# Kernel tuning notes

Measured on AMD Instinct MI355X. Metric: run time of the kernel, lower is better.

## Reference

```python
import jax, jax.numpy as jnp
import numpy as np
from jax import lax

B, N, D, H, T = 32, 128, 512, 512, 31
INI = 0.01


def setup_inputs() -> dict:
    key = jax.random.key(0)
    ks = jax.random.split(key, 16)
    xav_dh = float(np.sqrt(2.0 / (D + H)))
    xav_hh = float(np.sqrt(2.0 / (H + H)))
    u = lambda k, s, a: jax.random.uniform(k, s, jnp.float32, -a, a)
    return {
        "attn_mem": jax.random.normal(ks[0], (B, N, D), jnp.float32),
        "mem_sizes": jax.random.randint(ks[1], (B,), 64, N + 1),
        "lstm_in": jax.random.normal(ks[2], (B, T, D), jnp.float32),
        "init_h": u(ks[3], (1, H), INI),
        "init_c": u(ks[4], (1, H), INI),
        "init_i": u(ks[5], (D,), 0.1),
        "w_ih": jax.random.normal(ks[6], (4 * H, D), jnp.float32) * xav_dh,
        "w_hh": jax.random.normal(ks[7], (4 * H, H), jnp.float32) * xav_hh,
        "b_ih": u(ks[8], (4 * H,), INI),
        "b_hh": u(ks[9], (4 * H,), INI),
        "attn_wm": jax.random.normal(ks[10], (D, H), jnp.float32) * xav_dh,
        "attn_wq": jax.random.normal(ks[11], (H, H), jnp.float32) * xav_hh,
        "attn_v": u(ks[12], (H,), INI),
        "hop_wm": jax.random.normal(ks[13], (D, H), jnp.float32) * xav_dh,
        "hop_wq": jax.random.normal(ks[14], (H, H), jnp.float32) * xav_hh,
        "hop_v": u(ks[15], (H,), INI),
    }


def _attention_score(feat, query, v, w):
    # feat: [B,N,H], query: [B,Tq,H] -> [B,Tq,N]
    q = jnp.einsum("bth,hk->btk", query, w)
    s = jnp.tanh(feat[:, None, :, :] + q[:, :, None, :])  # [B,Tq,N,H]
    return jnp.einsum("btnh,h->btn", s, v)


def _attention(feat, query, v, w, mask):
    score = _attention_score(feat, query, v, w)
    score = jnp.where(mask[:, None, :], score, -1e18)
    norm = jax.nn.softmax(score, axis=-1)
    return jnp.einsum("btn,bnh->bth", norm, feat)


def _lstm(x, h0, c0, w_ih, w_hh, b_ih, b_hh):
    # x: [T,B,D]; h0,c0: [B,H]; pytorch gate order i,f,g,o
    def step(carry, xt):
        h, c = carry
        g = xt @ w_ih.T + h @ w_hh.T + b_ih + b_hh
        i, f, gg, o = jnp.split(g, 4, axis=-1)
        c = jax.nn.sigmoid(f) * c + jax.nn.sigmoid(i) * jnp.tanh(gg)
        h = jax.nn.sigmoid(o) * jnp.tanh(c)
        return (h, c), h
    _, ys = lax.scan(step, (h0, c0), x)
    return ys  # [T,B,H]


def reference(attn_mem, mem_sizes, lstm_in, init_h, init_c, init_i,
              w_ih, w_hh, b_ih, b_hh, attn_wm, attn_wq, attn_v,
              hop_wm, hop_wq, hop_v, n_hop=1):
    bs, n, d = attn_mem.shape
    attn_feat = attn_mem @ attn_wm  # [B,N,H]
    hop_feat = attn_mem @ hop_wm   # [B,N,H]
    h0 = jnp.broadcast_to(init_h[0], (bs, init_h.shape[1]))
    c0 = jnp.broadcast_to(init_c[0], (bs, init_c.shape[1]))
    x = jnp.concatenate([jnp.broadcast_to(init_i, (bs, 1, d)), lstm_in], axis=1)
    query = _lstm(jnp.transpose(x, (1, 0, 2)), h0, c0, w_ih, w_hh, b_ih, b_hh)
    query = jnp.transpose(query, (1, 0, 2))  # [B,Tq,H]
    mask = jnp.arange(n)[None, :] < mem_sizes[:, None]  # [B,N]
    for _ in range(n_hop):
        query = _attention(hop_feat, query, hop_v, hop_wq, mask)
    return _attention_score(attn_feat, query, attn_v, attn_wq)
```

## Files before the change

kernel.cpp:

```cpp
#include <hip/hip_runtime.h>

typedef unsigned short u16;
typedef unsigned long long u64;
typedef __bf16 bf16x8 __attribute__((ext_vector_type(8)));
typedef float f32x4 __attribute__((ext_vector_type(4)));

__device__ __forceinline__ float b2f(u16 u) {
    unsigned int x = ((unsigned int)u) << 16;
    return __builtin_bit_cast(float, x);
}
__device__ __forceinline__ u16 f2b(float f) {
    unsigned int u = __builtin_bit_cast(unsigned int, f);
    unsigned int r = (u + 0x7FFFu + ((u >> 16) & 1u)) >> 16;
    return (u16)r;
}
__device__ __forceinline__ unsigned int pack2(float a, float b) {
    return (unsigned int)f2b(a) | ((unsigned int)f2b(b) << 16);
}
__device__ __forceinline__ float fast_rcp(float x) { return __builtin_amdgcn_rcpf(x); }
__device__ __forceinline__ float fast_tanh(float x) {
    float e = __expf(2.f * x);
    return 1.f - 2.f * fast_rcp(e + 1.f);
}
__device__ __forceinline__ float fast_sig(float x) {
    float e = __expf(-x);
    return fast_rcp(1.f + e);
}

#define FLAG_STRIDE 32

__launch_bounds__(256)
__global__ void k_prep(const float* __restrict__ attn_mem, u16* __restrict__ amem_bf,
                       const float* __restrict__ w_ih, u16* __restrict__ wih_bf,
                       const float* __restrict__ w_hh, u16* __restrict__ whh_bf,
                       const float* __restrict__ lstm_in, const float* __restrict__ init_i,
                       u16* __restrict__ xfull,
                       const float* s0, const float* s1, const float* s2, const float* s3,
                       u16* d0, u16* d1, u16* d2, u16* d3,
                       unsigned int* __restrict__ flags) {
    __shared__ float tile[32][33];
    int bid = blockIdx.x;
    int tid = threadIdx.x;
    if (bid == 0 && tid < 64)
        __hip_atomic_store(&flags[tid * FLAG_STRIDE], 0u, __ATOMIC_RELAXED,
                           __HIP_MEMORY_SCOPE_AGENT);
    if (bid < 4096) {
        const float* s;
        u16* d;
        int i;
        if (bid < 2048) { s = attn_mem; d = amem_bf; i = bid * 256 + tid; }
        else if (bid < 3072) { s = w_ih; d = wih_bf; i = (bid - 2048) * 256 + tid; }
        else { s = w_hh; d = whh_bf; i = (bid - 3072) * 256 + tid; }
        float4 a = ((const float4*)s)[i];
        uint2 p;
        p.x = pack2(a.x, a.y);
        p.y = pack2(a.z, a.w);
        ((uint2*)d)[i] = p;
    } else if (bid < 4608) {
        int idx = (bid - 4096) * 256 + tid;
        int c = idx & 127;
        int t = (idx >> 7) & 31;
        int b = idx >> 12;
        const float4* src = (t == 0) ? ((const float4*)init_i) + c
                                     : ((const float4*)lstm_in) + ((b * 31 + (t - 1)) * 128 + c);
        float4 a = *src;
        uint2 p;
        p.x = pack2(a.x, a.y);
        p.y = pack2(a.z, a.w);
        ((uint2*)xfull)[idx] = p;
    } else {
        int local = bid - 4608;
        int z = local >> 8, rem = local & 255;
        int by = (rem >> 4) * 32, bx = (rem & 15) * 32;
        const float* s;
        u16* d;
        switch (z) {
            case 0: s = s0; d = d0; break;
            case 1: s = s1; d = d1; break;
            case 2: s = s2; d = d2; break;
            default: s = s3; d = d3; break;
        }
        int tx = tid & 31, ty = tid >> 5;
        for (int i = 0; i < 32; i += 8) tile[ty + i][tx] = s[(by + ty + i) * 512 + bx + tx];
        __syncthreads();
        for (int i = 0; i < 32; i += 8) d[(bx + ty + i) * 512 + by + tx] = f2b(tile[tx][ty + i]);
    }
}

template <bool BF16OUT>
__launch_bounds__(256)
__global__ void k_gemm(const u16* __restrict__ A, const u16* __restrict__ Bt,
                       void* __restrict__ Cv, int GN,
                       const float* __restrict__ bias1, const float* __restrict__ bias2) {
    __shared__ u16 As[64][40];
    __shared__ u16 Bs[64][40];
    int m0 = blockIdx.y * 64, n0 = blockIdx.x * 64;
    int tid = threadIdx.x;
    int lane = tid & 63, w = tid >> 6;
    int wm = w >> 1, wn = w & 1;
    int l15 = lane & 15, quad = lane >> 4;
    f32x4 acc[2][2] = {};
    int ar = tid >> 2, ac = (tid & 3) * 8;
    const u16* Ap = A + (m0 + ar) * 512 + ac;
    const u16* Bp = Bt + (n0 + ar) * 512 + ac;
    for (int kt = 0; kt < 16; ++kt) {
        uint4 av = *(const uint4*)(Ap + kt * 32);
        uint4 bv = *(const uint4*)(Bp + kt * 32);
        __syncthreads();
        *(uint4*)&As[ar][ac] = av;
        *(uint4*)&Bs[ar][ac] = bv;
        __syncthreads();
        bf16x8 a0 = *(const bf16x8*)&As[wm * 32 + l15][quad * 8];
        bf16x8 a1 = *(const bf16x8*)&As[wm * 32 + 16 + l15][quad * 8];
        bf16x8 b0 = *(const bf16x8*)&Bs[wn * 32 + l15][quad * 8];
        bf16x8 b1 = *(const bf16x8*)&Bs[wn * 32 + 16 + l15][quad * 8];
        acc[0][0] = __builtin_amdgcn_mfma_f32_16x16x32_bf16(a0, b0, acc[0][0], 0, 0, 0);
        acc[0][1] = __builtin_amdgcn_mfma_f32_16x16x32_bf16(a0, b1, acc[0][1], 0, 0, 0);
        acc[1][0] = __builtin_amdgcn_mfma_f32_16x16x32_bf16(a1, b0, acc[1][0], 0, 0, 0);
        acc[1][1] = __builtin_amdgcn_mfma_f32_16x16x32_bf16(a1, b1, acc[1][1], 0, 0, 0);
    }
    for (int ai = 0; ai < 2; ++ai)
        for (int bi = 0; bi < 2; ++bi) {
            int row = m0 + wm * 32 + ai * 16 + quad * 4;
            int col = n0 + wn * 32 + bi * 16 + l15;
            float bias = 0.f;
            if (bias1) bias = bias1[col] + bias2[col];
            if constexpr (BF16OUT) {
                u16* C = (u16*)Cv;
                for (int r = 0; r < 4; ++r) C[(row + r) * GN + col] = f2b(acc[ai][bi][r] + bias);
            } else {
                float* C = (float*)Cv;
                for (int r = 0; r < 4; ++r) C[(row + r) * GN + col] = acc[ai][bi][r] + bias;
            }
        }
}

__launch_bounds__(256)
__global__ void k_feat(const u16* __restrict__ A,
                       const u16* __restrict__ B0, const u16* __restrict__ B1,
                       u16* __restrict__ C0, u16* __restrict__ C1) {
    __shared__ u16 As[64][40];
    __shared__ u16 Bs[64][40];
    int by = blockIdx.y;
    const u16* Bt;
    u16* C;
    int m0;
    if (by < 64) { Bt = B0; C = C0; m0 = by * 64; }
    else { Bt = B1; C = C1; m0 = (by - 64) * 64; }
    int n0 = blockIdx.x * 64;
    int tid = threadIdx.x;
    int lane = tid & 63, w = tid >> 6;
    int wm = w >> 1, wn = w & 1;
    int l15 = lane & 15, quad = lane >> 4;
    f32x4 acc[2][2] = {};
    int ar = tid >> 2, ac = (tid & 3) * 8;
    const u16* Ap = A + (m0 + ar) * 512 + ac;
    const u16* Bp = Bt + (n0 + ar) * 512 + ac;
    for (int kt = 0; kt < 16; ++kt) {
        uint4 av = *(const uint4*)(Ap + kt * 32);
        uint4 bv = *(const uint4*)(Bp + kt * 32);
        __syncthreads();
        *(uint4*)&As[ar][ac] = av;
        *(uint4*)&Bs[ar][ac] = bv;
        __syncthreads();
        bf16x8 a0 = *(const bf16x8*)&As[wm * 32 + l15][quad * 8];
        bf16x8 a1 = *(const bf16x8*)&As[wm * 32 + 16 + l15][quad * 8];
        bf16x8 b0 = *(const bf16x8*)&Bs[wn * 32 + l15][quad * 8];
        bf16x8 b1 = *(const bf16x8*)&Bs[wn * 32 + 16 + l15][quad * 8];
        acc[0][0] = __builtin_amdgcn_mfma_f32_16x16x32_bf16(a0, b0, acc[0][0], 0, 0, 0);
        acc[0][1] = __builtin_amdgcn_mfma_f32_16x16x32_bf16(a0, b1, acc[0][1], 0, 0, 0);
        acc[1][0] = __builtin_amdgcn_mfma_f32_16x16x32_bf16(a1, b0, acc[1][0], 0, 0, 0);
        acc[1][1] = __builtin_amdgcn_mfma_f32_16x16x32_bf16(a1, b1, acc[1][1], 0, 0, 0);
    }
    for (int ai = 0; ai < 2; ++ai)
        for (int bi = 0; bi < 2; ++bi) {
            int row = m0 + wm * 32 + ai * 16 + quad * 4;
            int col = n0 + wn * 32 + bi * 16 + l15;
            for (int r = 0; r < 4; ++r) C[(row + r) * 512 + col] = f2b(acc[ai][bi][r]);
        }
}

__launch_bounds__(256, 1)
__global__ void k_lstm2(const u16* __restrict__ w_hh_bf, const float* __restrict__ xw,
                        const float* __restrict__ init_h, const float* __restrict__ init_c,
                        u16* __restrict__ query, u64* __restrict__ hbuf,
                        unsigned int* __restrict__ flags) {
    __shared__ u16 Bw[32][520];
    __shared__ u16 Ah[32][520];
    __shared__ float gl[32][33];
    __shared__ u16 gbuf[32][8];
    int tid = threadIdx.x;
    int k0 = blockIdx.x * 8;
    int lane = tid & 63, w = tid >> 6;
    int mi = w >> 1, ni = w & 1;
    int l15 = lane & 15, quad = lane >> 4;
    int row = tid >> 3, seg = tid & 7;
    {
        int j = (row >> 3) * 512 + k0 + (row & 7);
        const uint4* src = (const uint4*)(w_hh_bf + j * 512);
        for (int i = 0; i < 8; ++i)
            *(uint4*)&Bw[row][(seg + 8 * i) * 8] = src[seg + 8 * i];
    }
    for (int i = 0; i < 8; ++i) {
        int col = (seg + 8 * i) * 8;
        float4 f0 = *(const float4*)(init_h + col);
        float4 f1 = *(const float4*)(init_h + col + 4);
        uint4 p;
        p.x = pack2(f0.x, f0.y);
        p.y = pack2(f0.z, f0.w);
        p.z = pack2(f1.x, f1.y);
        p.w = pack2(f1.z, f1.w);
        *(uint4*)&Ah[row][col] = p;
    }
    float c = init_c[k0 + seg];
    float xcur0, xcur1, xcur2, xcur3;
    {
        const float* p = xw + (row << 5) * 2048 + k0 + seg;
        xcur0 = p[0]; xcur1 = p[512]; xcur2 = p[1024]; xcur3 = p[1536];
    }
    __syncthreads();
    for (int t = 0; t < 32; ++t) {
        f32x4 acc = {};
#pragma unroll
        for (int kc = 0; kc < 16; ++kc) {
            bf16x8 a = *(const bf16x8*)&Ah[mi * 16 + l15][kc * 32 + quad * 8];
            bf16x8 b = *(const bf16x8*)&Bw[ni * 16 + l15][kc * 32 + quad * 8];
            acc = __builtin_amdgcn_mfma_f32_16x16x32_bf16(a, b, acc, 0, 0, 0);
        }
        {
            int r0 = mi * 16 + quad * 4, col = ni * 16 + l15;
            for (int r = 0; r < 4; ++r) gl[r0 + r][col] = acc[r];
        }
        __syncthreads();
        int b = row, kg = k0 + seg;
        float gi = gl[b][seg] + xcur0;
        float gf = gl[b][8 + seg] + xcur1;
        float gg = gl[b][16 + seg] + xcur2;
        float go = gl[b][24 + seg] + xcur3;
        float cnew = fast_sig(gf) * c + fast_sig(gi) * fast_tanh(gg);
        c = cnew;
        float h = fast_sig(go) * fast_tanh(cnew);
        u16 hb = f2b(h);
        if (t == 31) {
            query[((b << 5) + t) * 512 + kg] = hb;
            break;
        }
        gbuf[b][seg] = hb;
        __syncthreads();
        if (tid < 64) {
            int b2 = tid >> 1, half = tid & 1;
            u64 v = *(const u64*)&gbuf[b2][half * 4];
            u64* dst = hbuf + (t & 1) * 4096 + blockIdx.x * 64 + tid;
            __hip_atomic_store(dst, v, __ATOMIC_RELAXED, __HIP_MEMORY_SCOPE_AGENT);
            __builtin_amdgcn_s_waitcnt(0);
            if (tid == 0)
                __hip_atomic_store(&flags[blockIdx.x * FLAG_STRIDE], (unsigned int)(t + 1),
                                   __ATOMIC_RELAXED, __HIP_MEMORY_SCOPE_AGENT);
            while (true) {
                unsigned int f = __hip_atomic_load(&flags[tid * FLAG_STRIDE],
                                                   __ATOMIC_RELAXED, __HIP_MEMORY_SCOPE_AGENT);
                if (__ballot(f > (unsigned int)t) == ~0ull) break;
                __builtin_amdgcn_s_sleep(1);
            }
        }
        __syncthreads();
        query[((b << 5) + t) * 512 + kg] = hb;
        float xn0, xn1, xn2, xn3;
        {
            const float* p = xw + ((row << 5) + (t + 1)) * 2048 + k0 + seg;
            xn0 = p[0]; xn1 = p[512]; xn2 = p[1024]; xn3 = p[1536];
        }
        {
            const u64* src = hbuf + (t & 1) * 4096;
#pragma unroll
            for (int i = 0; i < 8; ++i) {
                int bid2 = seg + 8 * i;
                u64 v0 = __hip_atomic_load(&src[bid2 * 64 + row * 2], __ATOMIC_RELAXED,
                                           __HIP_MEMORY_SCOPE_AGENT);
                u64 v1 = __hip_atomic_load(&src[bid2 * 64 + row * 2 + 1], __ATOMIC_RELAXED,
                                           __HIP_MEMORY_SCOPE_AGENT);
                *(u64*)&Ah[row][bid2 * 8] = v0;
                *(u64*)&Ah[row][bid2 * 8 + 4] = v1;
            }
        }
        __syncthreads();
        xcur0 = xn0; xcur1 = xn1; xcur2 = xn2; xcur3 = xn3;
    }
}

__launch_bounds__(256)
__global__ void k_hop(const u16* __restrict__ feat, const float* __restrict__ q,
                      const float* __restrict__ v, const int* __restrict__ mem_sizes,
                      u16* __restrict__ nq) {
    __shared__ float qs[512];
    __shared__ float vs[512];
    __shared__ float sc[128];
    __shared__ float ns[128];
    int bt = blockIdx.x;
    int b = bt >> 5;
    int tid = threadIdx.x;
    qs[tid] = q[bt * 512 + tid];
    qs[tid + 256] = q[bt * 512 + 256 + tid];
    vs[tid] = v[tid];
    vs[tid + 256] = v[tid + 256];
    __syncthreads();
    int lane = tid & 63, w = tid >> 6;
    int h0 = lane * 8;
    float qv[8], vv[8];
#pragma unroll
    for (int i = 0; i < 8; ++i) { qv[i] = qs[h0 + i]; vv[i] = vs[h0 + i]; }
    const u16* fb = feat + (size_t)b * 128 * 512;
    for (int i = 0; i < 32; ++i) {
        int n = w * 32 + i;
        uint4 fv = *(const uint4*)(fb + n * 512 + h0);
        float fr[8];
        fr[0] = b2f((u16)(fv.x & 0xFFFF)); fr[1] = b2f((u16)(fv.x >> 16));
        fr[2] = b2f((u16)(fv.y & 0xFFFF)); fr[3] = b2f((u16)(fv.y >> 16));
        fr[4] = b2f((u16)(fv.z & 0xFFFF)); fr[5] = b2f((u16)(fv.z >> 16));
        fr[6] = b2f((u16)(fv.w & 0xFFFF)); fr[7] = b2f((u16)(fv.w >> 16));
        float a = 0.f;
#pragma unroll
        for (int jj = 0; jj < 8; ++jj) a += fast_tanh(fr[jj] + qv[jj]) * vv[jj];
        for (int off = 1; off < 64; off <<= 1) a += __shfl_xor(a, off);
        if (lane == 0) sc[n] = a;
    }
    __syncthreads();
    if (tid < 64) {
        int ms = mem_sizes[b];
        float s0 = (tid < ms) ? sc[tid] : -1e30f;
        float s1 = (tid + 64 < ms) ? sc[tid + 64] : -1e30f;
        float m = fmaxf(s0, s1);
        for (int off = 1; off < 64; off <<= 1) m = fmaxf(m, __shfl_xor(m, off));
        float e0 = __expf(s0 - m), e1 = __expf(s1 - m);
        float s = e0 + e1;
        for (int off = 1; off < 64; off <<= 1) s += __shfl_xor(s, off);
        float r = fast_rcp(s);
        ns[tid] = e0 * r;
        ns[tid + 64] = e1 * r;
    }
    __syncthreads();
    float a0 = 0.f, a1 = 0.f;
    int hc = tid * 2;
    for (int n = 0; n < 128; ++n) {
        float f = ns[n];
        unsigned int pv = *(const unsigned int*)(fb + n * 512 + hc);
        a0 += f * b2f((u16)(pv & 0xFFFF));
        a1 += f * b2f((u16)(pv >> 16));
    }
    ((unsigned int*)nq)[bt * 256 + tid] = pack2(a0, a1);
}

__launch_bounds__(256)
__global__ void k_score(const u16* __restrict__ feat, const float* __restrict__ q,
                        const float* __restrict__ v, float* __restrict__ outp) {
    __shared__ float qs[512];
    __shared__ float vs[512];
    __shared__ float sc[128];
    int bt = blockIdx.x;
    int b = bt >> 5;
    int tid = threadIdx.x;
    qs[tid] = q[bt * 512 + tid];
    qs[tid + 256] = q[bt * 512 + 256 + tid];
    vs[tid] = v[tid];
    vs[tid + 256] = v[tid + 256];
    __syncthreads();
    int lane = tid & 63, w = tid >> 6;
    int h0 = lane * 8;
    float qv[8], vv[8];
#pragma unroll
    for (int i = 0; i < 8; ++i) { qv[i] = qs[h0 + i]; vv[i] = vs[h0 + i]; }
    const u16* fb = feat + (size_t)b * 128 * 512;
    for (int i = 0; i < 32; ++i) {
        int n = w * 32 + i;
        uint4 fv = *(const uint4*)(fb + n * 512 + h0);
        float fr[8];
        fr[0] = b2f((u16)(fv.x & 0xFFFF)); fr[1] = b2f((u16)(fv.x >> 16));
        fr[2] = b2f((u16)(fv.y & 0xFFFF)); fr[3] = b2f((u16)(fv.y >> 16));
        fr[4] = b2f((u16)(fv.z & 0xFFFF)); fr[5] = b2f((u16)(fv.z >> 16));
        fr[6] = b2f((u16)(fv.w & 0xFFFF)); fr[7] = b2f((u16)(fv.w >> 16));
        float a = 0.f;
#pragma unroll
        for (int jj = 0; jj < 8; ++jj) a += fast_tanh(fr[jj] + qv[jj]) * vv[jj];
        for (int off = 1; off < 64; off <<= 1) a += __shfl_xor(a, off);
        if (lane == 0) sc[n] = a;
    }
    __syncthreads();
    if (tid < 128) outp[bt * 128 + tid] = sc[tid];
}

extern "C" void kernel_launch(void* const* d_in, const int* in_sizes, int n_in,
                              void* d_out, int out_size, void* d_ws, size_t ws_size,
                              hipStream_t stream) {
    (void)in_sizes; (void)n_in; (void)out_size; (void)ws_size;
    const float* attn_mem = (const float*)d_in[0];
    const int* mem_sizes = (const int*)d_in[1];
    const float* lstm_in = (const float*)d_in[2];
    const float* init_h = (const float*)d_in[3];
    const float* init_c = (const float*)d_in[4];
    const float* init_i = (const float*)d_in[5];
    const float* w_ih = (const float*)d_in[6];
    const float* w_hh = (const float*)d_in[7];
    const float* b_ih = (const float*)d_in[8];
    const float* b_hh = (const float*)d_in[9];
    const float* attn_wm = (const float*)d_in[10];
    const float* attn_wq = (const float*)d_in[11];
    const float* attn_v = (const float*)d_in[12];
    const float* hop_wm = (const float*)d_in[13];
    const float* hop_wq = (const float*)d_in[14];
    const float* hop_v = (const float*)d_in[15];
    float* out = (float*)d_out;

    char* ws = (char*)d_ws;
    size_t off = 0;
    auto alloc = [&](size_t bytes) {
        void* p = ws + off;
        off += (bytes + 255) & ~(size_t)255;
        return p;
    };
    u16* amem_bf = (u16*)alloc(4096 * 512 * 2);
    u16* xfull_bf = (u16*)alloc(1024 * 512 * 2);
    u16* wih_bf = (u16*)alloc(2048 * 512 * 2);
    u16* whh_bf = (u16*)alloc(2048 * 512 * 2);
    u16* WmT_hop = (u16*)alloc(512 * 512 * 2);
    u16* WmT_attn = (u16*)alloc(512 * 512 * 2);
    u16* WqT_hop = (u16*)alloc(512 * 512 * 2);
    u16* WqT_attn = (u16*)alloc(512 * 512 * 2);
    float* xw = (float*)alloc(1024 * 2048 * 4);
    u16* hop_feat = (u16*)alloc(4096 * 512 * 2);
    u16* attn_feat = (u16*)alloc(4096 * 512 * 2);
    u16* query = (u16*)alloc(1024 * 512 * 2);
    u64* hbuf = (u64*)alloc(2 * 64 * 64 * 8);
    unsigned int* flags = (unsigned int*)alloc(64 * FLAG_STRIDE * 4);
    float* qbuf = (float*)alloc(1024 * 512 * 4);
    u16* nq = (u16*)alloc(1024 * 512 * 2);

    k_prep<<<5632, 256, 0, stream>>>(attn_mem, amem_bf, w_ih, wih_bf, w_hh, whh_bf,
                                     lstm_in, init_i, xfull_bf,
                                     attn_wm, hop_wm, hop_wq, attn_wq,
                                     WmT_attn, WmT_hop, WqT_hop, WqT_attn, flags);
    k_gemm<false><<<dim3(32, 16), 256, 0, stream>>>(xfull_bf, wih_bf, xw, 2048, b_ih, b_hh);
    k_feat<<<dim3(8, 128), 256, 0, stream>>>(amem_bf, WmT_hop, WmT_attn, hop_feat, attn_feat);
    k_lstm2<<<64, 256, 0, stream>>>(whh_bf, xw, init_h, init_c, query, hbuf, flags);
    k_gemm<false><<<dim3(8, 16), 256, 0, stream>>>(query, WqT_hop, qbuf, 512, nullptr, nullptr);
    k_hop<<<1024, 256, 0, stream>>>(hop_feat, qbuf, hop_v, mem_sizes, nq);
    k_gemm<false><<<dim3(8, 16), 256, 0, stream>>>(nq, WqT_attn, qbuf, 512, nullptr, nullptr);
    k_score<<<1024, 256, 0, stream>>>(attn_feat, qbuf, attn_v, out);
}
```

Baseline: 337.9 us.

## Merge input GEMMs into one launch and fuse hop query projection into LSTM

The x@W_ih GEMM and the two feature GEMMs are merged into one kernel launch with a flat block index. The hop query projection (h @ Wq_hop) moves into the persistent LSTM kernel. Two idle waves compute the previous step's projection with MFMA while wave 0 spins on the cross-block flag, and the last step is handled after the loop. This removes two kernel launches and the round trip of the bf16 query buffer, at the cost of extra LDS and per-step MFMA work inside the latency-bound recurrence.

```diff
diff --git a/kernel.cpp b/kernel.cpp
--- a/kernel.cpp
+++ b/kernel.cpp
@@ -1,6 +1,7 @@
 #include <hip/hip_runtime.h>
 
 typedef unsigned short u16;
+typedef unsigned int u32;
 typedef unsigned long long u64;
 typedef __bf16 bf16x8 __attribute__((ext_vector_type(8)));
 typedef float f32x4 __attribute__((ext_vector_type(4)));
@@ -87,6 +88,69 @@
     }
 }
 
+__launch_bounds__(256)
+__global__ void k_mid(const u16* __restrict__ xfull, const u16* __restrict__ wih,
+                      float* __restrict__ xw,
+                      const float* __restrict__ b_ih, const float* __restrict__ b_hh,
+                      const u16* __restrict__ amem,
+                      const u16* __restrict__ WmT_hop, const u16* __restrict__ WmT_attn,
+                      u16* __restrict__ hop_feat, u16* __restrict__ attn_feat) {
+    __shared__ u16 As[64][40];
+    __shared__ u16 Bs[64][40];
+    int id = blockIdx.x;
+    const u16 *A, *Bt;
+    float* Cf = nullptr;
+    u16* Cb = nullptr;
+    const float *bias1 = nullptr, *bias2 = nullptr;
+    int m0, n0, GN;
+    if (id < 512) {
+        A = xfull; Bt = wih; GN = 2048;
+        m0 = (id >> 5) * 64; n0 = (id & 31) * 64;
+        Cf = xw; bias1 = b_ih; bias2 = b_hh;
+    } else {
+        int local = id - 512;
+        A = amem; GN = 512;
+        if (local < 512) { Bt = WmT_hop; Cb = hop_feat; }
+        else { Bt = WmT_attn; Cb = attn_feat; local -= 512; }
+        m0 = (local >> 3) * 64; n0 = (local & 7) * 64;
+    }
+    int tid = threadIdx.x;
+    int lane = tid & 63, w = tid >> 6;
+    int wm = w >> 1, wn = w & 1;
+    int l15 = lane & 15, quad = lane >> 4;
+    f32x4 acc[2][2] = {};
+    int ar = tid >> 2, ac = (tid & 3) * 8;
+    const u16* Ap = A + (m0 + ar) * 512 + ac;
+    const u16* Bp = Bt + (n0 + ar) * 512 + ac;
+    for (int kt = 0; kt < 16; ++kt) {
+        uint4 av = *(const uint4*)(Ap + kt * 32);
+        uint4 bv = *(const uint4*)(Bp + kt * 32);
+        __syncthreads();
+        *(uint4*)&As[ar][ac] = av;
+        *(uint4*)&Bs[ar][ac] = bv;
+        __syncthreads();
+        bf16x8 a0 = *(const bf16x8*)&As[wm * 32 + l15][quad * 8];
+        bf16x8 a1 = *(const bf16x8*)&As[wm * 32 + 16 + l15][quad * 8];
+        bf16x8 b0 = *(const bf16x8*)&Bs[wn * 32 + l15][quad * 8];
+        bf16x8 b1 = *(const bf16x8*)&Bs[wn * 32 + 16 + l15][quad * 8];
+        acc[0][0] = __builtin_amdgcn_mfma_f32_16x16x32_bf16(a0, b0, acc[0][0], 0, 0, 0);
+        acc[0][1] = __builtin_amdgcn_mfma_f32_16x16x32_bf16(a0, b1, acc[0][1], 0, 0, 0);
+        acc[1][0] = __builtin_amdgcn_mfma_f32_16x16x32_bf16(a1, b0, acc[1][0], 0, 0, 0);
+        acc[1][1] = __builtin_amdgcn_mfma_f32_16x16x32_bf16(a1, b1, acc[1][1], 0, 0, 0);
+    }
+    for (int ai = 0; ai < 2; ++ai)
+        for (int bi = 0; bi < 2; ++bi) {
+            int row = m0 + wm * 32 + ai * 16 + quad * 4;
+            int col = n0 + wn * 32 + bi * 16 + l15;
+            if (Cb) {
+                for (int r = 0; r < 4; ++r) Cb[(row + r) * GN + col] = f2b(acc[ai][bi][r]);
+            } else {
+                float bias = bias1[col] + bias2[col];
+                for (int r = 0; r < 4; ++r) Cf[(row + r) * GN + col] = acc[ai][bi][r] + bias;
+            }
+        }
+}
+
 template <bool BF16OUT>
 __launch_bounds__(256)
 __global__ void k_gemm(const u16* __restrict__ A, const u16* __restrict__ Bt,
@@ -135,60 +199,16 @@
         }
 }
 
-__launch_bounds__(256)
-__global__ void k_feat(const u16* __restrict__ A,
-                       const u16* __restrict__ B0, const u16* __restrict__ B1,
-                       u16* __restrict__ C0, u16* __restrict__ C1) {
-    __shared__ u16 As[64][40];
-    __shared__ u16 Bs[64][40];
-    int by = blockIdx.y;
-    const u16* Bt;
-    u16* C;
-    int m0;
-    if (by < 64) { Bt = B0; C = C0; m0 = by * 64; }
-    else { Bt = B1; C = C1; m0 = (by - 64) * 64; }
-    int n0 = blockIdx.x * 64;
-    int tid = threadIdx.x;
-    int lane = tid & 63, w = tid >> 6;
-    int wm = w >> 1, wn = w & 1;
-    int l15 = lane & 15, quad = lane >> 4;
-    f32x4 acc[2][2] = {};
-    int ar = tid >> 2, ac = (tid & 3) * 8;
-    const u16* Ap = A + (m0 + ar) * 512 + ac;
-    const u16* Bp = Bt + (n0 + ar) * 512 + ac;
-    for (int kt = 0; kt < 16; ++kt) {
-        uint4 av = *(const uint4*)(Ap + kt * 32);
-        uint4 bv = *(const uint4*)(Bp + kt * 32);
-        __syncthreads();
-        *(uint4*)&As[ar][ac] = av;
-        *(uint4*)&Bs[ar][ac] = bv;
-        __syncthreads();
-        bf16x8 a0 = *(const bf16x8*)&As[wm * 32 + l15][quad * 8];
-        bf16x8 a1 = *(const bf16x8*)&As[wm * 32 + 16 + l15][quad * 8];
-        bf16x8 b0 = *(const bf16x8*)&Bs[wn * 32 + l15][quad * 8];
-        bf16x8 b1 = *(const bf16x8*)&Bs[wn * 32 + 16 + l15][quad * 8];
-        acc[0][0] = __builtin_amdgcn_mfma_f32_16x16x32_bf16(a0, b0, acc[0][0], 0, 0, 0);
-        acc[0][1] = __builtin_amdgcn_mfma_f32_16x16x32_bf16(a0, b1, acc[0][1], 0, 0, 0);
-        acc[1][0] = __builtin_amdgcn_mfma_f32_16x16x32_bf16(a1, b0, acc[1][0], 0, 0, 0);
-        acc[1][1] = __builtin_amdgcn_mfma_f32_16x16x32_bf16(a1, b1, acc[1][1], 0, 0, 0);
-    }
-    for (int ai = 0; ai < 2; ++ai)
-        for (int bi = 0; bi < 2; ++bi) {
-            int row = m0 + wm * 32 + ai * 16 + quad * 4;
-            int col = n0 + wn * 32 + bi * 16 + l15;
-            for (int r = 0; r < 4; ++r) C[(row + r) * 512 + col] = f2b(acc[ai][bi][r]);
-        }
-}
-
 __launch_bounds__(256, 1)
-__global__ void k_lstm2(const u16* __restrict__ w_hh_bf, const float* __restrict__ xw,
+__global__ void k_lstm4(const u16* __restrict__ w_hh_bf, const float* __restrict__ xw,
                         const float* __restrict__ init_h, const float* __restrict__ init_c,
-                        u16* __restrict__ query, u64* __restrict__ hbuf,
-                        unsigned int* __restrict__ flags) {
+                        const u16* __restrict__ wq_hop_T, float* __restrict__ qbuf,
+                        u64* __restrict__ hbuf, unsigned int* __restrict__ flags) {
     __shared__ u16 Bw[32][520];
     __shared__ u16 Ah[32][520];
     __shared__ float gl[32][33];
     __shared__ u16 gbuf[32][8];
+    __shared__ u16 Wq[16][520];
     int tid = threadIdx.x;
     int k0 = blockIdx.x * 8;
     int lane = tid & 63, w = tid >> 6;
@@ -201,6 +221,17 @@
         for (int i = 0; i < 8; ++i)
             *(uint4*)&Bw[row][(seg + 8 * i) * 8] = src[seg + 8 * i];
     }
+    if (row < 16) {
+        if (row < 8) {
+            const uint4* src = (const uint4*)(wq_hop_T + (k0 + row) * 512);
+            for (int i = 0; i < 8; ++i)
+                *(uint4*)&Wq[row][(seg + 8 * i) * 8] = src[seg + 8 * i];
+        } else {
+            uint4 z = {0, 0, 0, 0};
+            for (int i = 0; i < 8; ++i)
+                *(uint4*)&Wq[row][(seg + 8 * i) * 8] = z;
+        }
+    }
     for (int i = 0; i < 8; ++i) {
         int col = (seg + 8 * i) * 8;
         float4 f0 = *(const float4*)(init_h + col);
@@ -241,10 +272,6 @@
         c = cnew;
         float h = fast_sig(go) * fast_tanh(cnew);
         u16 hb = f2b(h);
-        if (t == 31) {
-            query[((b << 5) + t) * 512 + kg] = hb;
-            break;
-        }
         gbuf[b][seg] = hb;
         __syncthreads();
         if (tid < 64) {
@@ -262,12 +289,26 @@
                 if (__ballot(f > (unsigned int)t) == ~0ull) break;
                 __builtin_amdgcn_s_sleep(1);
             }
-        }
-        __syncthreads();
-        query[((b << 5) + t) * 512 + kg] = hb;
+        } else if (t > 0 && w <= 2) {
+            int mt = w - 1;
+            f32x4 acc2 = {};
+#pragma unroll
+            for (int kc = 0; kc < 16; ++kc) {
+                bf16x8 a = *(const bf16x8*)&Ah[mt * 16 + l15][kc * 32 + quad * 8];
+                bf16x8 bq = *(const bf16x8*)&Wq[l15][kc * 32 + quad * 8];
+                acc2 = __builtin_amdgcn_mfma_f32_16x16x32_bf16(a, bq, acc2, 0, 0, 0);
+            }
+            if (l15 < 8) {
+                int bidx = mt * 16 + quad * 4;
+                for (int r = 0; r < 4; ++r)
+                    qbuf[(((bidx + r) << 5) + (t - 1)) * 512 + k0 + l15] = acc2[r];
+            }
+        }
+        __syncthreads();
+        int tn = (t < 31) ? t + 1 : 31;
         float xn0, xn1, xn2, xn3;
         {
-            const float* p = xw + ((row << 5) + (t + 1)) * 2048 + k0 + seg;
+            const float* p = xw + ((row << 5) + tn) * 2048 + k0 + seg;
             xn0 = p[0]; xn1 = p[512]; xn2 = p[1024]; xn3 = p[1536];
         }
         {
@@ -285,6 +326,21 @@
         }
         __syncthreads();
         xcur0 = xn0; xcur1 = xn1; xcur2 = xn2; xcur3 = xn3;
+    }
+    if (w == 1 || w == 2) {
+        int mt = w - 1;
+        f32x4 acc2 = {};
+#pragma unroll
+        for (int kc = 0; kc < 16; ++kc) {
+            bf16x8 a = *(const bf16x8*)&Ah[mt * 16 + l15][kc * 32 + quad * 8];
+            bf16x8 bq = *(const bf16x8*)&Wq[l15][kc * 32 + quad * 8];
+            acc2 = __builtin_amdgcn_mfma_f32_16x16x32_bf16(a, bq, acc2, 0, 0, 0);
+        }
+        if (l15 < 8) {
+            int bidx = mt * 16 + quad * 4;
+            for (int r = 0; r < 4; ++r)
+                qbuf[(((bidx + r) << 5) + 31) * 512 + k0 + l15] = acc2[r];
+        }
     }
 }
 
@@ -428,7 +484,6 @@
     float* xw = (float*)alloc(1024 * 2048 * 4);
     u16* hop_feat = (u16*)alloc(4096 * 512 * 2);
     u16* attn_feat = (u16*)alloc(4096 * 512 * 2);
-    u16* query = (u16*)alloc(1024 * 512 * 2);
     u64* hbuf = (u64*)alloc(2 * 64 * 64 * 8);
     unsigned int* flags = (unsigned int*)alloc(64 * FLAG_STRIDE * 4);
     float* qbuf = (float*)alloc(1024 * 512 * 4);
@@ -438,10 +493,9 @@
                                      lstm_in, init_i, xfull_bf,
                                      attn_wm, hop_wm, hop_wq, attn_wq,
                                      WmT_attn, WmT_hop, WqT_hop, WqT_attn, flags);
-    k_gemm<false><<<dim3(32, 16), 256, 0, stream>>>(xfull_bf, wih_bf, xw, 2048, b_ih, b_hh);
-    k_feat<<<dim3(8, 128), 256, 0, stream>>>(amem_bf, WmT_hop, WmT_attn, hop_feat, attn_feat);
-    k_lstm2<<<64, 256, 0, stream>>>(whh_bf, xw, init_h, init_c, query, hbuf, flags);
-    k_gemm<false><<<dim3(8, 16), 256, 0, stream>>>(query, WqT_hop, qbuf, 512, nullptr, nullptr);
+    k_mid<<<1536, 256, 0, stream>>>(xfull_bf, wih_bf, xw, b_ih, b_hh,
+                                    amem_bf, WmT_hop, WmT_attn, hop_feat, attn_feat);
+    k_lstm4<<<64, 256, 0, stream>>>(whh_bf, xw, init_h, init_c, WqT_hop, qbuf, hbuf, flags);
     k_hop<<<1024, 256, 0, stream>>>(hop_feat, qbuf, hop_v, mem_sizes, nq);
     k_gemm<false><<<dim3(8, 16), 256, 0, stream>>>(nq, WqT_attn, qbuf, 512, nullptr, nullptr);
     k_score<<<1024, 256, 0, stream>>>(attn_feat, qbuf, attn_v, out);
```

Result: no change. 332.5 us (-1.6%).
